# Kernel tuning notes

Hardware: AMD Instinct MI355X
Metric: run time of the kernel (lower is better)

The kernel has to match this reference:

```python
import jax, jax.numpy as jnp
import numpy as np

TEMP = 0.5  # RelaxedBernoulli temperature
EPS = 1e-6


def setup_inputs() -> dict:
    B, T, D = 8, 2048, 512
    key = jax.random.key(0)
    kx, ku, k1, k2 = jax.random.split(key, 4)
    x = jax.random.normal(kx, (B, T, D), dtype=jnp.float32)
    u = jax.random.uniform(ku, (B, T), dtype=jnp.float32, minval=EPS, maxval=1.0 - EPS)
    # upstream linear initialized to identity (per module __init__)
    W_up = jnp.eye(D, dtype=jnp.float32)
    s = 1.0 / np.sqrt(D)
    W1 = jax.random.normal(k1, (D, D), dtype=jnp.float32) * s
    b1 = jnp.zeros((D,), dtype=jnp.float32)
    W2 = jax.random.normal(k2, (1, D), dtype=jnp.float32) * s
    b2 = jnp.zeros((1,), dtype=jnp.float32)  # init_bias = 0.0
    return {"x": x, "u": u, "W_up": W_up, "W1": W1, "b1": b1, "W2": W2, "b2": b2}


def reference(x, u, W_up, W1, b1, W2, b2):
    B, T, D = x.shape
    # upstream linear (no bias); torch Linear computes x @ W^T
    hidden = jnp.einsum('btd,ed->bte', x, W_up)
    # boundary MLP: Linear -> GELU(exact) -> Linear(out=1), then sigmoid
    h = jax.nn.gelu(jnp.einsum('btd,ed->bte', hidden, W1) + b1, approximate=False)
    logits = jnp.einsum('btd,od->bto', h, W2)[..., 0] + b2[0]  # [B,T]
    probs = jax.nn.sigmoid(logits)
    # RelaxedBernoulli rsample with explicit uniform noise u (straight-through hard)
    p = jnp.clip(probs, EPS, 1.0 - EPS)
    uu = jnp.clip(u, EPS, 1.0 - EPS)
    soft = jax.nn.sigmoid((jnp.log(p) - jnp.log1p(-p) + jnp.log(uu) - jnp.log1p(-uu)) / TEMP)
    hard = jax.lax.stop_gradient((soft > 0.5).astype(x.dtype))
    boundaries = hard + soft - jax.lax.stop_gradient(soft)
    # guarantee at least one boundary per row (set last frame to 1.0)
    row_sum = jnp.sum(jax.lax.stop_gradient(boundaries), axis=1)
    boundaries = boundaries.at[:, -1].set(jnp.where(row_sum == 0, 1.0, boundaries[:, -1]))
    # mean pooling over segments; segments padded to S = T (static upper bound)
    S = T
    seg_id = jnp.cumsum(boundaries, axis=1) - boundaries  # hh1 in original, [B,T]
    foo = jnp.arange(S, dtype=x.dtype)[None, None, :] - seg_id[:, :, None]  # [B,T,S]
    in_seg = jax.lax.stop_gradient(foo) == 0
    soft_mask = jnp.where(in_seg, 1.0 - foo, 0.0)  # value 1 where in segment, grad -d(foo)
    counts = jnp.clip(jnp.sum(soft_mask, axis=1), 1e-8, None)  # [B,S]
    seg_sum = jnp.einsum('bts,btd->bsd', soft_mask, hidden)  # bmm mean-pool
    pooled = seg_sum / counts[:, :, None]  # rows past true n_segments are zero
    return pooled, boundaries, probs, hidden
```

## Files before the change

### kernel.cpp

```cpp
#include <hip/hip_runtime.h>
#include <cstdint>
#include <cstddef>

typedef _Float16 half8 __attribute__((ext_vector_type(8)));
typedef float floatx4 __attribute__((ext_vector_type(4)));

constexpr int Bc = 8, Tc = 2048, Dc = 512;
constexpr float kSplitScale = 2048.0f;
constexpr float kInvSplit   = 4.8828125e-4f;
constexpr float kF16MinNorm = 6.103515625e-5f;

__device__ __forceinline__ void split8(const float* __restrict__ in, _Float16* __restrict__ hi,
                                       _Float16* __restrict__ lo, int i)
{
    const float4* ip = reinterpret_cast<const float4*>(in) + 2 * i;
    float4 a = ip[0], b = ip[1];
    float v[8] = {a.x, a.y, a.z, a.w, b.x, b.y, b.z, b.w};
    half8 h, l;
#pragma unroll
    for (int e = 0; e < 8; ++e) {
        float hv = (fabsf(v[e]) >= kF16MinNorm) ? (float)(_Float16)v[e] : 0.0f;
        h[e] = (_Float16)hv;
        l[e] = (_Float16)((v[e] - hv) * kSplitScale);
    }
    reinterpret_cast<half8*>(hi)[i] = h;
    reinterpret_cast<half8*>(lo)[i] = l;
}

__global__ __launch_bounds__(256)
void split_kernel(const float* __restrict__ in, _Float16* __restrict__ hi,
                  _Float16* __restrict__ lo, int n8)
{
    int i = blockIdx.x * 256 + threadIdx.x;
    if (i >= n8) return;
    split8(in, hi, lo, i);
}

__global__ __launch_bounds__(256)
void split3_kernel(const float* __restrict__ x,  _Float16* __restrict__ xh,  _Float16* __restrict__ xl,  int nx8,
                   const float* __restrict__ wu, _Float16* __restrict__ wuh, _Float16* __restrict__ wul, int nw8,
                   const float* __restrict__ w1, _Float16* __restrict__ w1h, _Float16* __restrict__ w1l)
{
    int i = blockIdx.x * 256 + threadIdx.x;
    if (i < nx8) { split8(x, xh, xl, i); return; }
    i -= nx8;
    if (i < nw8) { split8(wu, wuh, wul, i); return; }
    i -= nw8;
    if (i < nw8) { split8(w1, w1h, w1l, i); return; }
}

template<bool LOGITS>
__global__ __launch_bounds__(256)
void mfma_gemm(const _Float16* __restrict__ Ah, const _Float16* __restrict__ Al,
               const _Float16* __restrict__ Bh, const _Float16* __restrict__ Bl,
               float* __restrict__ C, const float* __restrict__ bias,
               const float* __restrict__ w2, float* __restrict__ logits,
               int M, int N, int K)
{
    __shared__ _Float16 As[2][128 * 64];
    __shared__ _Float16 Bs[2][128 * 64];
    const int t = threadIdx.x;
    const int bm = blockIdx.x * 128;
    const int bn = blockIdx.y * 128;
    const int lane = t & 63;
    const int wid = t >> 6;
    const int wr = (wid >> 1) * 64;
    const int wc = (wid & 1) * 64;
    const int rr = lane >> 3;
    const int ss = lane & 7;
    const int gchunk = (ss ^ rr) * 8;

    floatx4 acc[4][4];
#pragma unroll
    for (int i = 0; i < 4; ++i)
#pragma unroll
        for (int j = 0; j < 4; ++j) acc[i][j] = floatx4{0.f, 0.f, 0.f, 0.f};

    auto stage = [&](int st) {
        const int c  = st >> 3;
        const int k0 = (st & 7) << 6;
        const _Float16* Asrc = (c == 1) ? Al : Ah;
        const _Float16* Bsrc = (c == 0) ? Bl : Bh;
        _Float16* Ad = As[st & 1];
        _Float16* Bd = Bs[st & 1];
#pragma unroll
        for (int i = 0; i < 4; ++i) {
            const int rbase = i * 32 + wid * 8;
            __builtin_amdgcn_global_load_lds(
                (const __attribute__((address_space(1))) void*)
                    (Asrc + (size_t)(bm + rbase + rr) * K + k0 + gchunk),
                (__attribute__((address_space(3))) void*)(Ad + rbase * 64),
                16, 0, 0);
            __builtin_amdgcn_global_load_lds(
                (const __attribute__((address_space(1))) void*)
                    (Bsrc + (size_t)(bn + rbase + rr) * K + k0 + gchunk),
                (__attribute__((address_space(3))) void*)(Bd + rbase * 64),
                16, 0, 0);
        }
    };

    stage(0);
    __syncthreads();

#pragma unroll 2
    for (int st = 0; st < 24; ++st) {
        if (st < 23) stage(st + 1);
        const char* Ab = reinterpret_cast<const char*>(As[st & 1]);
        const char* Bb = reinterpret_cast<const char*>(Bs[st & 1]);
#pragma unroll
        for (int kk = 0; kk < 2; ++kk) {
            half8 af[4], bf[4];
            const int kb = kk * 64 + ((lane >> 4) * 16);
#pragma unroll
            for (int i = 0; i < 4; ++i) {
                const int rowa = wr + i * 16 + (lane & 15);
                af[i] = *reinterpret_cast<const half8*>(Ab + rowa * 128 + (kb ^ ((rowa & 7) * 16)));
                const int rowb = wc + i * 16 + (lane & 15);
                bf[i] = *reinterpret_cast<const half8*>(Bb + rowb * 128 + (kb ^ ((rowb & 7) * 16)));
            }
#pragma unroll
            for (int i = 0; i < 4; ++i)
#pragma unroll
                for (int j = 0; j < 4; ++j)
                    acc[i][j] = __builtin_amdgcn_mfma_f32_16x16x32_f16(af[i], bf[j], acc[i][j], 0, 0, 0);
        }
        if (st == 15) {
#pragma unroll
            for (int i = 0; i < 4; ++i)
#pragma unroll
                for (int j = 0; j < 4; ++j)
#pragma unroll
                    for (int r = 0; r < 4; ++r) acc[i][j][r] *= kInvSplit;
        }
        __syncthreads();
    }

    if (!LOGITS) {
#pragma unroll
        for (int i = 0; i < 4; ++i) {
            const int m = bm + wr + i * 16 + ((lane >> 4) * 4);
#pragma unroll
            for (int j = 0; j < 4; ++j) {
                const int n = bn + wc + j * 16 + (lane & 15);
#pragma unroll
                for (int r = 0; r < 4; ++r)
                    C[(size_t)(m + r) * N + n] = acc[i][j][r];
            }
        }
    } else {
        float b1v[4], w2v[4];
#pragma unroll
        for (int j = 0; j < 4; ++j) {
            const int n = bn + wc + j * 16 + (lane & 15);
            b1v[j] = bias[n];
            w2v[j] = w2[n];
        }
#pragma unroll
        for (int i = 0; i < 4; ++i) {
            float part[4] = {0.f, 0.f, 0.f, 0.f};
#pragma unroll
            for (int j = 0; j < 4; ++j)
#pragma unroll
                for (int r = 0; r < 4; ++r) {
                    const float v = acc[i][j][r] + b1v[j];
                    const float g = 0.5f * v * (1.0f + erff(v * 0.70710678118654752f));
                    part[r] += g * w2v[j];
                }
#pragma unroll
            for (int r = 0; r < 4; ++r) {
                float p = part[r];
                p += __shfl_xor(p, 1);
                p += __shfl_xor(p, 2);
                p += __shfl_xor(p, 4);
                p += __shfl_xor(p, 8);
                if ((lane & 15) == 0) {
                    const int m = bm + wr + i * 16 + ((lane >> 4) * 4) + r;
                    atomicAdd(&logits[m], p);
                }
            }
        }
    }
}

__global__ __launch_bounds__(256)
void probs_bnd_kernel(const float* __restrict__ logits, const float* __restrict__ b2,
                      const float* __restrict__ u, float* __restrict__ probs,
                      float* __restrict__ bnd, int n)
{
    int i = blockIdx.x * 256 + threadIdx.x;
    if (i >= n) return;
    const float lg = logits[i] + b2[0];
    const float p = 1.0f / (1.0f + expf(-lg));
    probs[i] = p;
    const float pc = fminf(fmaxf(p, 1e-6f), 1.0f - 1e-6f);
    const float uu = fminf(fmaxf(u[i], 1e-6f), 1.0f - 1e-6f);
    const float z = (logf(pc) - log1pf(-pc) + logf(uu) - log1pf(-uu)) * 2.0f;
    bnd[i] = (z > 0.0f) ? 1.0f : 0.0f;
}

__global__ __launch_bounds__(64)
void scan_fix(float* __restrict__ bnd, int* __restrict__ starts, float* __restrict__ counts)
{
    __shared__ float cnt[Tc];
    const int b = blockIdx.x;
    const int lane = threadIdx.x;
    constexpr int CH = Tc / 64;
    float* rb = bnd + (size_t)b * Tc;
    float v[CH];
    int lsum = 0;
#pragma unroll
    for (int j = 0; j < CH; ++j) { v[j] = rb[lane * CH + j]; lsum += (v[j] > 0.5f); }
    int tot = lsum;
#pragma unroll
    for (int off = 32; off >= 1; off >>= 1) tot += __shfl_xor(tot, off);
    const float prevLast = __shfl_up(v[CH - 1], 1);
    if (tot == 0 && lane == 63) { v[CH - 1] = 1.0f; rb[Tc - 1] = 1.0f; }
    int incl = lsum;
#pragma unroll
    for (int off = 1; off < 64; off <<= 1) {
        const int nv = __shfl_up(incl, off);
        if (lane >= off) incl += nv;
    }
    int run = incl - lsum;
    for (int s = lane; s < Tc; s += 64) cnt[s] = 0.0f;
    __syncthreads();
    float prev = (lane == 0) ? 1.0f : prevLast;
#pragma unroll
    for (int j = 0; j < CH; ++j) {
        const int t_ = lane * CH + j;
        if (prev > 0.5f) starts[(size_t)b * Tc + run] = t_;
        atomicAdd(&cnt[run], 1.0f);
        run += (v[j] > 0.5f);
        prev = v[j];
    }
    __syncthreads();
    for (int s = lane; s < Tc; s += 64) counts[(size_t)b * Tc + s] = cnt[s];
}

__global__ __launch_bounds__(128)
void pool_kernel(const float* __restrict__ hidden, const int* __restrict__ starts,
                 const float* __restrict__ counts, float* __restrict__ pooled)
{
    const int blk = blockIdx.x;
    const int b = blk >> 11;
    float4* outp = reinterpret_cast<float4*>(pooled + (size_t)blk * Dc) + threadIdx.x;
    const float c = counts[blk];
    if (c < 0.5f) { *outp = float4{0.f, 0.f, 0.f, 0.f}; return; }
    const int len = (int)c;
    const int start = starts[blk];
    const float4* hp = reinterpret_cast<const float4*>(
                           hidden + ((size_t)(b << 11) + start) * Dc) + threadIdx.x;
    double s0 = 0, s1 = 0, s2 = 0, s3 = 0;
    for (int r = 0; r < len; ++r) {
        const float4 v = hp[(size_t)r * (Dc / 4)];
        s0 += v.x; s1 += v.y; s2 += v.z; s3 += v.w;
    }
    const double inv = 1.0 / (double)len;
    *outp = float4{(float)(s0 * inv), (float)(s1 * inv), (float)(s2 * inv), (float)(s3 * inv)};
}

extern "C" void kernel_launch(void* const* d_in, const int* in_sizes, int n_in,
                              void* d_out, int out_size, void* d_ws, size_t ws_size,
                              hipStream_t stream)
{
    const float* x   = (const float*)d_in[0];
    const float* u   = (const float*)d_in[1];
    const float* Wup = (const float*)d_in[2];
    const float* W1  = (const float*)d_in[3];
    const float* b1  = (const float*)d_in[4];
    const float* W2  = (const float*)d_in[5];
    const float* b2  = (const float*)d_in[6];

    float* out = (float*)d_out;
    const size_t MT = (size_t)Bc * Tc;
    const size_t pooledN = MT * Dc;
    float* pooled = out;
    float* bnd    = out + pooledN;
    float* probs  = bnd + MT;
    float* hidden = probs + MT;

    _Float16* xh = (_Float16*)pooled;
    _Float16* xl = xh + pooledN;
    _Float16* hh = xh;
    _Float16* hl = xl;

    char* ws = (char*)d_ws;
    _Float16* wuh = (_Float16*)ws;  ws += (size_t)Dc * Dc * 2;
    _Float16* wul = (_Float16*)ws;  ws += (size_t)Dc * Dc * 2;
    _Float16* w1h = (_Float16*)ws;  ws += (size_t)Dc * Dc * 2;
    _Float16* w1l = (_Float16*)ws;  ws += (size_t)Dc * Dc * 2;
    float* logits = (float*)ws;     ws += MT * 4;
    int*   starts = (int*)ws;       ws += MT * 4;
    float* counts = (float*)ws;     ws += MT * 4;

    const int M = (int)MT, N = Dc, K = Dc;
    const int nx8 = M * K / 8;
    const int nw8 = K * K / 8;

    split3_kernel<<<(nx8 + 2 * nw8 + 255) / 256, 256, 0, stream>>>(
        x, xh, xl, nx8, Wup, wuh, wul, nw8, W1, w1h, w1l);

    dim3 gg(M / 128, N / 128);
    mfma_gemm<false><<<gg, 256, 0, stream>>>(xh, xl, wuh, wul, hidden,
                                             nullptr, nullptr, nullptr, M, N, K);
    split_kernel<<<(nx8 + 255) / 256, 256, 0, stream>>>(hidden, hh, hl, nx8);
    hipMemsetAsync(logits, 0, MT * 4, stream);
    mfma_gemm<true><<<gg, 256, 0, stream>>>(hh, hl, w1h, w1l, nullptr,
                                            b1, W2, logits, M, N, K);
    probs_bnd_kernel<<<((int)MT + 255) / 256, 256, 0, stream>>>(logits, b2, u, probs, bnd, (int)MT);
    scan_fix<<<Bc, 64, 0, stream>>>(bnd, starts, counts);
    pool_kernel<<<(int)MT, 128, 0, stream>>>(hidden, starts, counts, pooled);
}
```

Before: 202.1 us.

## Fuse hidden split into GEMM epilogue and replace logit atomics with partial buffers

When the workspace is large enough, the first GEMM writes the fp16 hi/lo split of hidden directly in its epilogue, which removes the separate split kernel's re-read of hidden. The second GEMM writes per-column-slice partial logits into 8 buffers instead of doing atomicAdd into a memset buffer, so the memset is dropped. The probs/boundary kernel is folded into the scan kernel, which sums the partials itself. This trades extra epilogue stores and workspace use for fewer launches and less memory traffic, but probs and boundary computation now run inside only 8 blocks of 64 threads.

```diff
diff --git a/kernel.cpp b/kernel.cpp
--- a/kernel.cpp
+++ b/kernel.cpp
@@ -6,6 +6,7 @@
 typedef float floatx4 __attribute__((ext_vector_type(4)));
 
 constexpr int Bc = 8, Tc = 2048, Dc = 512;
+constexpr int MTOT = Bc * Tc;
 constexpr float kSplitScale = 2048.0f;
 constexpr float kInvSplit   = 4.8828125e-4f;
 constexpr float kF16MinNorm = 6.103515625e-5f;
@@ -53,9 +54,9 @@
 __global__ __launch_bounds__(256)
 void mfma_gemm(const _Float16* __restrict__ Ah, const _Float16* __restrict__ Al,
                const _Float16* __restrict__ Bh, const _Float16* __restrict__ Bl,
-               float* __restrict__ C, const float* __restrict__ bias,
-               const float* __restrict__ w2, float* __restrict__ logits,
-               int M, int N, int K)
+               float* __restrict__ C, _Float16* __restrict__ Ch, _Float16* __restrict__ Cl,
+               const float* __restrict__ bias, const float* __restrict__ w2,
+               float* __restrict__ part, int M, int N, int K)
 {
     __shared__ _Float16 As[2][128 * 64];
     __shared__ _Float16 Bs[2][128 * 64];
@@ -143,8 +144,16 @@
             for (int j = 0; j < 4; ++j) {
                 const int n = bn + wc + j * 16 + (lane & 15);
 #pragma unroll
-                for (int r = 0; r < 4; ++r)
-                    C[(size_t)(m + r) * N + n] = acc[i][j][r];
+                for (int r = 0; r < 4; ++r) {
+                    const float v = acc[i][j][r];
+                    const size_t idx = (size_t)(m + r) * N + n;
+                    C[idx] = v;
+                    if (Ch) {
+                        const float hv = (fabsf(v) >= kF16MinNorm) ? (float)(_Float16)v : 0.0f;
+                        Ch[idx] = (_Float16)hv;
+                        Cl[idx] = (_Float16)((v - hv) * kSplitScale);
+                    }
+                }
             }
         }
     } else {
@@ -155,66 +164,67 @@
             b1v[j] = bias[n];
             w2v[j] = w2[n];
         }
+        float* pp = part + (size_t)(blockIdx.y * 2 + (wid & 1)) * M;
 #pragma unroll
         for (int i = 0; i < 4; ++i) {
-            float part[4] = {0.f, 0.f, 0.f, 0.f};
+            float partial[4] = {0.f, 0.f, 0.f, 0.f};
 #pragma unroll
             for (int j = 0; j < 4; ++j)
 #pragma unroll
                 for (int r = 0; r < 4; ++r) {
                     const float v = acc[i][j][r] + b1v[j];
                     const float g = 0.5f * v * (1.0f + erff(v * 0.70710678118654752f));
-                    part[r] += g * w2v[j];
+                    partial[r] += g * w2v[j];
                 }
 #pragma unroll
             for (int r = 0; r < 4; ++r) {
-                float p = part[r];
+                float p = partial[r];
                 p += __shfl_xor(p, 1);
                 p += __shfl_xor(p, 2);
                 p += __shfl_xor(p, 4);
                 p += __shfl_xor(p, 8);
                 if ((lane & 15) == 0) {
                     const int m = bm + wr + i * 16 + ((lane >> 4) * 4) + r;
-                    atomicAdd(&logits[m], p);
+                    pp[m] = p;
                 }
             }
         }
     }
 }
 
-__global__ __launch_bounds__(256)
-void probs_bnd_kernel(const float* __restrict__ logits, const float* __restrict__ b2,
-                      const float* __restrict__ u, float* __restrict__ probs,
-                      float* __restrict__ bnd, int n)
-{
-    int i = blockIdx.x * 256 + threadIdx.x;
-    if (i >= n) return;
-    const float lg = logits[i] + b2[0];
-    const float p = 1.0f / (1.0f + expf(-lg));
-    probs[i] = p;
-    const float pc = fminf(fmaxf(p, 1e-6f), 1.0f - 1e-6f);
-    const float uu = fminf(fmaxf(u[i], 1e-6f), 1.0f - 1e-6f);
-    const float z = (logf(pc) - log1pf(-pc) + logf(uu) - log1pf(-uu)) * 2.0f;
-    bnd[i] = (z > 0.0f) ? 1.0f : 0.0f;
-}
-
 __global__ __launch_bounds__(64)
-void scan_fix(float* __restrict__ bnd, int* __restrict__ starts, float* __restrict__ counts)
+void scan_fix(const float* __restrict__ part, const float* __restrict__ b2,
+              const float* __restrict__ u, float* __restrict__ probs,
+              float* __restrict__ bnd, int* __restrict__ starts,
+              float* __restrict__ counts)
 {
     __shared__ float cnt[Tc];
     const int b = blockIdx.x;
     const int lane = threadIdx.x;
     constexpr int CH = Tc / 64;
-    float* rb = bnd + (size_t)b * Tc;
+    const size_t rowoff = (size_t)b * Tc;
+    const float bb = b2[0];
     float v[CH];
     int lsum = 0;
 #pragma unroll
-    for (int j = 0; j < CH; ++j) { v[j] = rb[lane * CH + j]; lsum += (v[j] > 0.5f); }
+    for (int j = 0; j < CH; ++j) {
+        const size_t gi = rowoff + lane * CH + j;
+        float lg = bb;
+#pragma unroll
+        for (int s = 0; s < 8; ++s) lg += part[(size_t)s * MTOT + gi];
+        const float p = 1.0f / (1.0f + expf(-lg));
+        probs[gi] = p;
+        const float pc = fminf(fmaxf(p, 1e-6f), 1.0f - 1e-6f);
+        const float uu = fminf(fmaxf(u[gi], 1e-6f), 1.0f - 1e-6f);
+        const float z = (logf(pc) - log1pf(-pc) + logf(uu) - log1pf(-uu)) * 2.0f;
+        v[j] = (z > 0.0f) ? 1.0f : 0.0f;
+        lsum += (v[j] > 0.5f);
+    }
     int tot = lsum;
 #pragma unroll
     for (int off = 32; off >= 1; off >>= 1) tot += __shfl_xor(tot, off);
     const float prevLast = __shfl_up(v[CH - 1], 1);
-    if (tot == 0 && lane == 63) { v[CH - 1] = 1.0f; rb[Tc - 1] = 1.0f; }
+    if (tot == 0 && lane == 63) v[CH - 1] = 1.0f;
     int incl = lsum;
 #pragma unroll
     for (int off = 1; off < 64; off <<= 1) {
@@ -228,13 +238,14 @@
 #pragma unroll
     for (int j = 0; j < CH; ++j) {
         const int t_ = lane * CH + j;
-        if (prev > 0.5f) starts[(size_t)b * Tc + run] = t_;
+        bnd[rowoff + t_] = v[j];
+        if (prev > 0.5f) starts[rowoff + run] = t_;
         atomicAdd(&cnt[run], 1.0f);
         run += (v[j] > 0.5f);
         prev = v[j];
     }
     __syncthreads();
-    for (int s = lane; s < Tc; s += 64) counts[(size_t)b * Tc + s] = cnt[s];
+    for (int s = lane; s < Tc; s += 64) counts[rowoff + s] = cnt[s];
 }
 
 __global__ __launch_bounds__(128)
@@ -272,7 +283,7 @@
     const float* b2  = (const float*)d_in[6];
 
     float* out = (float*)d_out;
-    const size_t MT = (size_t)Bc * Tc;
+    const size_t MT = (size_t)MTOT;
     const size_t pooledN = MT * Dc;
     float* pooled = out;
     float* bnd    = out + pooledN;
@@ -281,17 +292,19 @@
 
     _Float16* xh = (_Float16*)pooled;
     _Float16* xl = xh + pooledN;
-    _Float16* hh = xh;
-    _Float16* hl = xl;
 
     char* ws = (char*)d_ws;
+    const char* ws_end = (char*)d_ws + ws_size;
     _Float16* wuh = (_Float16*)ws;  ws += (size_t)Dc * Dc * 2;
     _Float16* wul = (_Float16*)ws;  ws += (size_t)Dc * Dc * 2;
     _Float16* w1h = (_Float16*)ws;  ws += (size_t)Dc * Dc * 2;
     _Float16* w1l = (_Float16*)ws;  ws += (size_t)Dc * Dc * 2;
-    float* logits = (float*)ws;     ws += MT * 4;
+    float* part   = (float*)ws;     ws += 8 * MT * 4;
     int*   starts = (int*)ws;       ws += MT * 4;
     float* counts = (float*)ws;     ws += MT * 4;
+    const bool fused_split = ((size_t)(ws_end - ws) >= 2 * pooledN * 2);
+    _Float16* hh = fused_split ? (_Float16*)ws : xh;
+    _Float16* hl = fused_split ? hh + pooledN : xl;
 
     const int M = (int)MT, N = Dc, K = Dc;
     const int nx8 = M * K / 8;
@@ -302,12 +315,13 @@
 
     dim3 gg(M / 128, N / 128);
     mfma_gemm<false><<<gg, 256, 0, stream>>>(xh, xl, wuh, wul, hidden,
+                                             fused_split ? hh : nullptr,
+                                             fused_split ? hl : nullptr,
                                              nullptr, nullptr, nullptr, M, N, K);
-    split_kernel<<<(nx8 + 255) / 256, 256, 0, stream>>>(hidden, hh, hl, nx8);
-    hipMemsetAsync(logits, 0, MT * 4, stream);
-    mfma_gemm<true><<<gg, 256, 0, stream>>>(hh, hl, w1h, w1l, nullptr,
-                                            b1, W2, logits, M, N, K);
-    probs_bnd_kernel<<<((int)MT + 255) / 256, 256, 0, stream>>>(logits, b2, u, probs, bnd, (int)MT);
-    scan_fix<<<Bc, 64, 0, stream>>>(bnd, starts, counts);
-    pool_kernel<<<(int)MT, 128, 0, stream>>>(hidden, starts, counts, pooled);
-}
+    if (!fused_split)
+        split_kernel<<<(nx8 + 255) / 256, 256, 0, stream>>>(hidden, hh, hl, nx8);
+    mfma_gemm<true><<<gg, 256, 0, stream>>>(hh, hl, w1h, w1l, nullptr, nullptr, nullptr,
+                                            b1, W2, part, M, N, K);
+    scan_fix<<<Bc, 64, 0, stream>>>(part, b2, u, probs, bnd, starts, counts);
+    pool_kernel<<<M, 128, 0, stream>>>(hidden, starts, counts, pooled);
+}
```

Result: slower. 217.0 us (+7.3%).
